# Kernel optimization log

Measured on AMD Instinct MI355X. Metric: run time of the kernel, lower is better.

## Reference

```python
import jax, jax.numpy as jnp
import numpy as np
import math

B, S, IN, H, M = 4, 2048, 256, 128, 128  # mem_dim must equal hidden_size


def _xavier(key, shape):
    fan_in, fan_out = shape[0], shape[-1]
    lim = math.sqrt(6.0 / (fan_in + fan_out))
    return jax.random.uniform(key, shape, jnp.float32, -lim, lim)


def setup_inputs() -> dict:
    key = jax.random.key(0)
    ks = jax.random.split(key, 8)
    return dict(
        x=jax.random.normal(ks[0], (B, S, IN), jnp.float32),
        c0=jnp.zeros((M, M), jnp.float32),   # init_hidden matrix memory
        n0=jnp.zeros((M, 1), jnp.float32),   # init_hidden normalizer
        w_q=_xavier(ks[1], (IN, H)), b_q=jnp.zeros((H,), jnp.float32),
        w_k=_xavier(ks[2], (IN, M)), b_k=jnp.zeros((M,), jnp.float32),
        w_v=_xavier(ks[3], (IN, M)), b_v=jnp.zeros((M,), jnp.float32),
        w_i=_xavier(ks[4], (IN, 1)), b_i=jnp.zeros((1,), jnp.float32),
        w_f=_xavier(ks[5], (IN, 1)), b_f=jnp.zeros((1,), jnp.float32),
        w_o=_xavier(ks[6], (IN, H)), b_o=jnp.zeros((H,), jnp.float32),
    )


def reference(x, c0, n0, w_q, b_q, w_k, b_k, w_v, b_v, w_i, b_i, w_f, b_f, w_o, b_o):
    Bb, Ss, Ii = x.shape
    Mm = w_k.shape[1]
    Hh = w_q.shape[1]
    xf = x.reshape(Bb * Ss, Ii)                                  # [N, IN]
    q = xf @ w_q + b_q                                           # [N, H]
    k = (xf @ w_k + b_k) * (1.0 / math.sqrt(Mm))                 # [N, M]
    v = xf @ w_v + b_v                                           # [N, M]
    i_t = jnp.exp(xf @ w_i + b_i)                                # [N, 1]
    f_t = jax.nn.sigmoid(xf @ w_f + b_f)                         # [N, 1]
    # Original loop never updates c_prev: c_t[n] = f[n]*c0 + i[n]*outer(v[n], k[n])
    c = f_t[:, :, None] * c0[None] + i_t[:, :, None] * (v[:, :, None] * k[:, None, :])  # [N, M, M]
    n = f_t[:, :, None] * n0[None] + i_t[:, :, None] * k[:, :, None]                    # [N, M, 1]
    c = c.reshape(Bb, Ss, Mm, Mm)
    n = n.reshape(Bb, Ss, Mm, 1)
    q4 = q.reshape(Bb, Ss, Hh)
    nq = jnp.einsum('bsm,bsm->bs', n[..., 0], q4)                # n^T q
    denom = jnp.maximum(jnp.abs(nq), 1.0)[..., None]             # max(|n^T q|, 1)
    h_tilde = jnp.einsum('bsmk,bsk->bsm', c, q4) / denom         # (c_t q) / denom
    o = jax.nn.sigmoid(xf @ w_o + b_o).reshape(Bb, Ss, Hh)
    h = o * h_tilde                                              # [B, S, H]
    return (h, c, n)
```

## Files before the change

kernel.cpp:

```cpp
#include <hip/hip_runtime.h>
#include <math.h>

#define B_    4
#define S_    2048
#define IN_   256
#define H_    128
#define M_    128
#define NROWS (B_ * S_)
#define RPB   16
#define TPB   256
#define XPAD  260

typedef float f4_t __attribute__((ext_vector_type(4)));

__global__ __launch_bounds__(TPB) void xlstm_proj(
    const float* __restrict__ x,
    const float* __restrict__ c0,
    const float* __restrict__ n0,
    const float* __restrict__ w_q, const float* __restrict__ b_q,
    const float* __restrict__ w_k, const float* __restrict__ b_k,
    const float* __restrict__ w_v, const float* __restrict__ b_v,
    const float* __restrict__ w_i, const float* __restrict__ b_i,
    const float* __restrict__ w_f, const float* __restrict__ b_f,
    const float* __restrict__ w_o, const float* __restrict__ b_o,
    float* __restrict__ out_h,
    float* __restrict__ out_n,
    float* __restrict__ kws,
    float* __restrict__ vws,
    float* __restrict__ ifws)
{
    __shared__ float xs[RPB][XPAD];
    __shared__ float qs[RPB][M_];
    __shared__ float ks[RPB][M_];
    __shared__ float vs[RPB][M_];
    __shared__ float os_[RPB][M_];
    __shared__ float itf[RPB][2];
    __shared__ float scal[RPB][2];

    const int t    = threadIdx.x;
    const int row0 = blockIdx.x * RPB;

    for (int p4 = t; p4 < RPB * IN_ / 4; p4 += TPB) {
        int p = p4 * 4;
        float4 v = *(const float4*)(x + (size_t)row0 * IN_ + p);
        int r = p >> 8, c = p & 255;
        *(float4*)&xs[r][c] = v;
    }
    __syncthreads();

    const int col   = t & 127;
    const int rbase = (t >> 7) * 8;

    {
        float accq[8], acck[8], accv[8], acco[8];
        #pragma unroll
        for (int r = 0; r < 8; ++r) { accq[r]=0.f; acck[r]=0.f; accv[r]=0.f; acco[r]=0.f; }

        #pragma unroll 2
        for (int k4 = 0; k4 < IN_; k4 += 4) {
            float4 xr[8];
            #pragma unroll
            for (int r = 0; r < 8; ++r) xr[r] = *(const float4*)&xs[rbase + r][k4];

            int wi = k4 * H_ + col;
            float4 wq, wk, wv, wo;
            wq.x = w_q[wi]; wq.y = w_q[wi + H_]; wq.z = w_q[wi + 2*H_]; wq.w = w_q[wi + 3*H_];
            wk.x = w_k[wi]; wk.y = w_k[wi + M_]; wk.z = w_k[wi + 2*M_]; wk.w = w_k[wi + 3*M_];
            wv.x = w_v[wi]; wv.y = w_v[wi + M_]; wv.z = w_v[wi + 2*M_]; wv.w = w_v[wi + 3*M_];
            wo.x = w_o[wi]; wo.y = w_o[wi + H_]; wo.z = w_o[wi + 2*H_]; wo.w = w_o[wi + 3*H_];

            #pragma unroll
            for (int r = 0; r < 8; ++r) {
                accq[r] = fmaf(xr[r].x, wq.x, fmaf(xr[r].y, wq.y, fmaf(xr[r].z, wq.z, fmaf(xr[r].w, wq.w, accq[r]))));
                acck[r] = fmaf(xr[r].x, wk.x, fmaf(xr[r].y, wk.y, fmaf(xr[r].z, wk.z, fmaf(xr[r].w, wk.w, acck[r]))));
                accv[r] = fmaf(xr[r].x, wv.x, fmaf(xr[r].y, wv.y, fmaf(xr[r].z, wv.z, fmaf(xr[r].w, wv.w, accv[r]))));
                acco[r] = fmaf(xr[r].x, wo.x, fmaf(xr[r].y, wo.y, fmaf(xr[r].z, wo.z, fmaf(xr[r].w, wo.w, acco[r]))));
            }
        }

        const float kscale = 0.08838834764831843f;
        #pragma unroll
        for (int r = 0; r < 8; ++r) {
            int row = rbase + r;
            qs[row][col]  = accq[r] + b_q[col];
            ks[row][col]  = (acck[r] + b_k[col]) * kscale;
            vs[row][col]  = accv[r] + b_v[col];
            float oo      = acco[r] + b_o[col];
            os_[row][col] = 1.f / (1.f + __expf(-oo));
        }
    }

    {
        const int gr = t >> 4, gseg = t & 15;
        const float* xrow = &xs[gr][gseg * 16];
        float pi = 0.f, pf = 0.f;
        #pragma unroll
        for (int u = 0; u < 4; ++u) {
            float4 xv  = *(const float4*)(xrow + u * 4);
            float4 wiv = *(const float4*)(w_i + gseg * 16 + u * 4);
            float4 wfv = *(const float4*)(w_f + gseg * 16 + u * 4);
            pi = fmaf(xv.x, wiv.x, fmaf(xv.y, wiv.y, fmaf(xv.z, wiv.z, fmaf(xv.w, wiv.w, pi))));
            pf = fmaf(xv.x, wfv.x, fmaf(xv.y, wfv.y, fmaf(xv.z, wfv.z, fmaf(xv.w, wfv.w, pf))));
        }
        #pragma unroll
        for (int m = 1; m < 16; m <<= 1) { pi += __shfl_xor(pi, m); pf += __shfl_xor(pf, m); }
        if (gseg == 0) {
            itf[gr][0] = __expf(pi + b_i[0]);
            itf[gr][1] = 1.f / (1.f + __expf(-(pf + b_f[0])));
        }
    }
    __syncthreads();

    float c0qr[8];
    {
        #pragma unroll
        for (int r = 0; r < 8; ++r) c0qr[r] = 0.f;
        const float* c0row = c0 + (size_t)col * M_;
        #pragma unroll 2
        for (int j4 = 0; j4 < M_; j4 += 4) {
            float4 w4 = *(const float4*)(c0row + j4);
            #pragma unroll
            for (int r = 0; r < 8; ++r) {
                float4 q4 = *(const float4*)&qs[rbase + r][j4];
                c0qr[r] = fmaf(w4.x, q4.x, fmaf(w4.y, q4.y, fmaf(w4.z, q4.z, fmaf(w4.w, q4.w, c0qr[r]))));
            }
        }
    }

    {
        const int gr = t >> 4, gseg = t & 15;
        const int j0 = gseg * 8;
        float pkq = 0.f, pnq = 0.f;
        #pragma unroll
        for (int u = 0; u < 2; ++u) {
            float4 kk = *(const float4*)&ks[gr][j0 + u * 4];
            float4 qq = *(const float4*)&qs[gr][j0 + u * 4];
            float4 nn = *(const float4*)(n0 + j0 + u * 4);
            pkq = fmaf(kk.x, qq.x, fmaf(kk.y, qq.y, fmaf(kk.z, qq.z, fmaf(kk.w, qq.w, pkq))));
            pnq = fmaf(nn.x, qq.x, fmaf(nn.y, qq.y, fmaf(nn.z, qq.z, fmaf(nn.w, qq.w, pnq))));
        }
        #pragma unroll
        for (int m = 1; m < 16; m <<= 1) { pkq += __shfl_xor(pkq, m); pnq += __shfl_xor(pnq, m); }
        if (gseg == 0) { scal[gr][0] = pkq; scal[gr][1] = pnq; }
    }
    __syncthreads();

    #pragma unroll
    for (int r = 0; r < 8; ++r) {
        int row = rbase + r;
        size_t grow = (size_t)(row0 + row);
        float iv = itf[row][0], fv = itf[row][1];
        float kv = ks[row][col];
        out_n[grow * M_ + col] = fmaf(fv, n0[col], iv * kv);
        float nq    = fmaf(fv, scal[row][1], iv * scal[row][0]);
        float denom = fmaxf(fabsf(nq), 1.0f);
        float ht = fmaf(fv, c0qr[r], iv * vs[row][col] * scal[row][0]) / denom;
        out_h[grow * H_ + col] = os_[row][col] * ht;
        kws[grow * M_ + col] = kv;
        vws[grow * M_ + col] = vs[row][col];
    }
    if (t < 32) {
        int r = t & 15;
        size_t grow = (size_t)(row0 + r);
        if (t < 16) ifws[grow * 2 + 0] = itf[r][0];
        else        ifws[grow * 2 + 1] = itf[r][1];
    }
}

__global__ __launch_bounds__(TPB) void xlstm_cstream(
    const float* __restrict__ c0,
    const float* __restrict__ kws,
    const float* __restrict__ vws,
    const float* __restrict__ ifws,
    float* __restrict__ out_c)
{
    const int t    = threadIdx.x;
    const int row0 = blockIdx.x * RPB;

    __shared__ float vsh[RPB][M_];
    __shared__ float ksh[RPB][M_];
    __shared__ float2 ish[RPB];

    for (int p4 = t; p4 < RPB * M_ / 4; p4 += TPB) {
        int idx = p4 * 4;
        int r = idx >> 7, c = idx & 127;
        *(float4*)&vsh[r][c] = *(const float4*)(vws + (size_t)row0 * M_ + idx);
        *(float4*)&ksh[r][c] = *(const float4*)(kws + (size_t)row0 * M_ + idx);
    }
    if (t < RPB) ish[t] = *(const float2*)(ifws + (size_t)(row0 + t) * 2);
    __syncthreads();

    const int base = t * 4;
    const int j    = base & 127;

    #pragma unroll 2
    for (int ch = 0; ch < 16; ++ch) {
        int p = (ch << 10) + base;
        int m = p >> 7;
        float4 c0v = *(const float4*)(c0 + p);
        #pragma unroll
        for (int r = 0; r < RPB; ++r) {
            float4 k4 = *(const float4*)&ksh[r][j];
            float  s  = ish[r].x * vsh[r][m];
            f4_t o4;
            o4.x = fmaf(ish[r].y, c0v.x, s * k4.x);
            o4.y = fmaf(ish[r].y, c0v.y, s * k4.y);
            o4.z = fmaf(ish[r].y, c0v.z, s * k4.z);
            o4.w = fmaf(ish[r].y, c0v.w, s * k4.w);
            __builtin_nontemporal_store(o4,
                (f4_t*)(out_c + (size_t)(row0 + r) * (M_ * M_) + p));
        }
    }
}

extern "C" void kernel_launch(void* const* d_in, const int* in_sizes, int n_in,
                              void* d_out, int out_size, void* d_ws, size_t ws_size,
                              hipStream_t stream) {
    const float* x   = (const float*)d_in[0];
    const float* c0  = (const float*)d_in[1];
    const float* n0  = (const float*)d_in[2];
    const float* w_q = (const float*)d_in[3];  const float* b_q = (const float*)d_in[4];
    const float* w_k = (const float*)d_in[5];  const float* b_k = (const float*)d_in[6];
    const float* w_v = (const float*)d_in[7];  const float* b_v = (const float*)d_in[8];
    const float* w_i = (const float*)d_in[9];  const float* b_i = (const float*)d_in[10];
    const float* w_f = (const float*)d_in[11]; const float* b_f = (const float*)d_in[12];
    const float* w_o = (const float*)d_in[13]; const float* b_o = (const float*)d_in[14];

    float* out   = (float*)d_out;
    float* out_h = out;
    float* out_c = out + (size_t)NROWS * H_;
    float* out_n = out_c + (size_t)NROWS * M_ * M_;

    float* kws  = (float*)d_ws;
    float* vws  = kws + (size_t)NROWS * M_;
    float* ifws = vws + (size_t)NROWS * M_;

    hipLaunchKernelGGL(xlstm_proj, dim3(NROWS / RPB), dim3(TPB), 0, stream,
                       x, c0, n0, w_q, b_q, w_k, b_k, w_v, b_v,
                       w_i, b_i, w_f, b_f, w_o, b_o,
                       out_h, out_n, kws, vws, ifws);

    hipLaunchKernelGGL(xlstm_cstream, dim3(NROWS / RPB), dim3(TPB), 0, stream,
                       c0, kws, vws, ifws, out_c);
}
```

Baseline: 147.8 us.

## Remap projection GEMM to per-matrix column groups with split-K across halves

```diff
diff --git a/kernel.cpp b/kernel.cpp
--- a/kernel.cpp
+++ b/kernel.cpp
@@ -48,45 +48,56 @@
     }
     __syncthreads();
 
-    const int col   = t & 127;
-    const int rbase = (t >> 7) * 8;
-
-    {
-        float accq[8], acck[8], accv[8], acco[8];
-        #pragma unroll
-        for (int r = 0; r < 8; ++r) { accq[r]=0.f; acck[r]=0.f; accv[r]=0.f; acco[r]=0.f; }
-
-        #pragma unroll 2
-        for (int k4 = 0; k4 < IN_; k4 += 4) {
-            float4 xr[8];
-            #pragma unroll
-            for (int r = 0; r < 8; ++r) xr[r] = *(const float4*)&xs[rbase + r][k4];
-
-            int wi = k4 * H_ + col;
-            float4 wq, wk, wv, wo;
-            wq.x = w_q[wi]; wq.y = w_q[wi + H_]; wq.z = w_q[wi + 2*H_]; wq.w = w_q[wi + 3*H_];
-            wk.x = w_k[wi]; wk.y = w_k[wi + M_]; wk.z = w_k[wi + 2*M_]; wk.w = w_k[wi + 3*M_];
-            wv.x = w_v[wi]; wv.y = w_v[wi + M_]; wv.z = w_v[wi + 2*M_]; wv.w = w_v[wi + 3*M_];
-            wo.x = w_o[wi]; wo.y = w_o[wi + H_]; wo.z = w_o[wi + 2*H_]; wo.w = w_o[wi + 3*H_];
-
-            #pragma unroll
-            for (int r = 0; r < 8; ++r) {
-                accq[r] = fmaf(xr[r].x, wq.x, fmaf(xr[r].y, wq.y, fmaf(xr[r].z, wq.z, fmaf(xr[r].w, wq.w, accq[r]))));
-                acck[r] = fmaf(xr[r].x, wk.x, fmaf(xr[r].y, wk.y, fmaf(xr[r].z, wk.z, fmaf(xr[r].w, wk.w, acck[r]))));
-                accv[r] = fmaf(xr[r].x, wv.x, fmaf(xr[r].y, wv.y, fmaf(xr[r].z, wv.z, fmaf(xr[r].w, wv.w, accv[r]))));
-                acco[r] = fmaf(xr[r].x, wo.x, fmaf(xr[r].y, wo.y, fmaf(xr[r].z, wo.z, fmaf(xr[r].w, wo.w, acco[r]))));
+    const int cg   = t & 31;
+    const int mat  = (t >> 5) & 3;
+    const int half = t >> 7;
+    const int c4   = cg * 4;
+
+    const float* W = (mat == 0) ? w_q : (mat == 1) ? w_k : (mat == 2) ? w_v : w_o;
+    float (*DST)[M_] = (mat == 0) ? qs : (mat == 1) ? ks : (mat == 2) ? vs : os_;
+
+    f4_t acc[16];
+    #pragma unroll
+    for (int r = 0; r < 16; ++r) acc[r] = (f4_t){0.f, 0.f, 0.f, 0.f};
+
+    const int k0base = half * 128;
+    #pragma unroll 2
+    for (int it = 0; it < 32; ++it) {
+        const int k0 = k0base + it * 4;
+        const float* wp = W + (size_t)k0 * H_ + c4;
+        f4_t w0 = *(const f4_t*)(wp);
+        f4_t w1 = *(const f4_t*)(wp + H_);
+        f4_t w2 = *(const f4_t*)(wp + 2 * H_);
+        f4_t w3 = *(const f4_t*)(wp + 3 * H_);
+
+        #pragma unroll
+        for (int r = 0; r < 16; ++r) {
+            f4_t xv = *(const f4_t*)&xs[r][k0];
+            acc[r] += xv.x * w0 + xv.y * w1 + xv.z * w2 + xv.w * w3;
+        }
+    }
+
+    if (half == 1) {
+        #pragma unroll
+        for (int r = 0; r < 16; ++r)
+            *(f4_t*)&DST[r][c4] = acc[r];
+    }
+    __syncthreads();
+    if (half == 0) {
+        const float kscale = 0.08838834764831843f;
+        const float* BIAS = (mat == 0) ? b_q : (mat == 1) ? b_k : (mat == 2) ? b_v : b_o;
+        f4_t b4 = *(const f4_t*)(BIAS + c4);
+        #pragma unroll
+        for (int r = 0; r < 16; ++r) {
+            f4_t s = acc[r] + *(const f4_t*)&DST[r][c4] + b4;
+            if (mat == 1) s *= kscale;
+            if (mat == 3) {
+                s.x = 1.f / (1.f + __expf(-s.x));
+                s.y = 1.f / (1.f + __expf(-s.y));
+                s.z = 1.f / (1.f + __expf(-s.z));
+                s.w = 1.f / (1.f + __expf(-s.w));
             }
-        }
-
-        const float kscale = 0.08838834764831843f;
-        #pragma unroll
-        for (int r = 0; r < 8; ++r) {
-            int row = rbase + r;
-            qs[row][col]  = accq[r] + b_q[col];
-            ks[row][col]  = (acck[r] + b_k[col]) * kscale;
-            vs[row][col]  = accv[r] + b_v[col];
-            float oo      = acco[r] + b_o[col];
-            os_[row][col] = 1.f / (1.f + __expf(-oo));
+            *(f4_t*)&DST[r][c4] = s;
         }
     }
 
@@ -111,6 +122,8 @@
     }
     __syncthreads();
 
+    const int col   = t & 127;
+    const int rbase = (t >> 7) * 8;
     float c0qr[8];
     {
         #pragma unroll
```

After: 152.9 us. 1.03x slower.
